# Kernel optimization log

Measured on AMD Instinct MI355X. Metric: run time of the kernel, lower is better.

## Reference

```python
import jax, jax.numpy as jnp
import numpy as np

N_NODES = 100000
N_EDGES = 1600000
N_GRAPHS = 256
IN_DIM, HID = 30, 40

def setup_inputs() -> dict:
    key = jax.random.key(0)
    ks = jax.random.split(key, 12)
    x = jax.random.normal(ks[0], (N_NODES, IN_DIM), dtype=jnp.float32)
    edge_index = jax.random.randint(ks[1], (2, N_EDGES), 0, N_NODES, dtype=jnp.int64)
    batch = jnp.sort(jax.random.randint(ks[2], (N_NODES,), 0, N_GRAPHS, dtype=jnp.int64))
    def glorot(k, shape):
        lim = float(np.sqrt(6.0 / (shape[0] + shape[1])))
        return jax.random.uniform(k, shape, dtype=jnp.float32, minval=-lim, maxval=lim)
    return {
        'x': x, 'edge_index': edge_index, 'batch': batch,
        'W1': glorot(ks[3], (IN_DIM, HID)), 'b1': jnp.zeros((HID,), jnp.float32),
        'W2': glorot(ks[4], (HID, HID)),    'b2': jnp.zeros((HID,), jnp.float32),
        'W3': glorot(ks[5], (HID, HID)),    'b3': jnp.zeros((HID,), jnp.float32),
        'lin_w': glorot(ks[6], (HID, 1)),   'lin_b': jnp.zeros((1,), jnp.float32),
    }

def _gcn_layer(x, src, dst, norm, W, b, n_nodes):
    # x: [N, Fin] -> [N, Fout]; fused gather-matmul-scatter form of GCNConv
    h = x @ W                                   # dense transform first (Fout small)
    msg = h[src] * norm[:, None]                # [E+N, Fout] gather + edge scale
    out = jax.ops.segment_sum(msg, dst, num_segments=n_nodes)
    return out + b

def reference(x, edge_index, batch, W1, b1, W2, b2, W3, b3, lin_w, lin_b):
    n = x.shape[0]
    loops = jnp.arange(n, dtype=edge_index.dtype)
    src = jnp.concatenate([edge_index[0], loops])  # add self loops (GCNConv default)
    dst = jnp.concatenate([edge_index[1], loops])
    deg = jax.ops.segment_sum(jnp.ones_like(dst, dtype=x.dtype), dst, num_segments=n)
    dinv = jax.lax.rsqrt(jnp.maximum(deg, 1.0))    # deg >= 1 thanks to self loops
    norm = dinv[src] * dinv[dst]

    h = jax.nn.relu(_gcn_layer(x, src, dst, norm, W1, b1, n))  # dropout inactive (eval)
    h = jax.nn.relu(_gcn_layer(h, src, dst, norm, W2, b2, n))
    h = jax.nn.relu(_gcn_layer(h, src, dst, norm, W3, b3, n))

    # global_mean_pool over graphs
    g_sum = jax.ops.segment_sum(h, batch, num_segments=N_GRAPHS)
    cnt = jax.ops.segment_sum(jnp.ones((n,), h.dtype), batch, num_segments=N_GRAPHS)
    g = g_sum / jnp.maximum(cnt, 1.0)[:, None]
    return g @ lin_w + lin_b                      # [N_GRAPHS, 1]
```

## Files before the change

### kernel.cpp

```cpp
#include <hip/hip_runtime.h>

#define HID 40
#define RBKT 196
#define BSH 9
#define CAP 12288
#define EPB 4096


__device__ inline unsigned pack2_bf16(float a, float b) {
    unsigned ua = __float_as_uint(a);
    unsigned ub = __float_as_uint(b);
    ua = (ua + 0x7fffu + ((ua >> 16) & 1u)) >> 16;
    ub = (ub + 0x7fffu + ((ub >> 16) & 1u)) & 0xffff0000u;
    return ua | ub;
}

__device__ inline void acc8_bf16(float* acc, uint4 v) {
    acc[0] += __uint_as_float(v.x << 16);
    acc[1] += __uint_as_float(v.x & 0xffff0000u);
    acc[2] += __uint_as_float(v.y << 16);
    acc[3] += __uint_as_float(v.y & 0xffff0000u);
    acc[4] += __uint_as_float(v.z << 16);
    acc[5] += __uint_as_float(v.z & 0xffff0000u);
    acc[6] += __uint_as_float(v.w << 16);
    acc[7] += __uint_as_float(v.w & 0xffff0000u);
}

__global__ void clear_kernel(int* __restrict__ bucket_cnt, float* __restrict__ g_sum, int G) {
    int t = blockIdx.x * blockDim.x + threadIdx.x;
    if (t < RBKT) bucket_cnt[t] = 0;
    if (t < G) g_sum[t] = 0.f;
}


__global__ __launch_bounds__(256) void binA_kernel(
        const int* __restrict__ esrc, const int* __restrict__ edst, int E,
        int* __restrict__ bucket_cnt, int* __restrict__ bucket_data) {
    __shared__ int cnt_l[RBKT];
    __shared__ int base_l[RBKT];
    int t = threadIdx.x;
    for (int b = t; b < RBKT; b += 256) cnt_l[b] = 0;
    __syncthreads();
    int e0 = blockIdx.x * EPB;
    int e1 = min(e0 + EPB, E);
    for (int e = e0 + t; e < e1; e += 256) {
        atomicAdd(&cnt_l[edst[e] >> BSH], 1);
    }
    __syncthreads();
    for (int b = t; b < RBKT; b += 256) {
        int c = cnt_l[b];
        base_l[b] = (c > 0) ? atomicAdd(&bucket_cnt[b], c) : 0;
        cnt_l[b] = 0;
    }
    __syncthreads();
    for (int e = e0 + t; e < e1; e += 256) {
        int d = edst[e];
        int s = esrc[e];
        int b = d >> BSH;
        int off = base_l[b] + atomicAdd(&cnt_l[b], 1);
        if (off < CAP) bucket_data[(size_t)b * CAP + off] = (s << BSH) | (d & 511);
    }
}

__global__ void scan_buckets_kernel(const int* __restrict__ cnt, int* __restrict__ base) {
    __shared__ int s[256];
    int t = threadIdx.x;
    int c = (t < RBKT) ? min(cnt[t], CAP) : 0;
    s[t] = c;
    __syncthreads();
    for (int off = 1; off < 256; off <<= 1) {
        int y = (t >= off) ? s[t - off] : 0;
        __syncthreads();
        s[t] += y;
        __syncthreads();
    }
    if (t < RBKT) base[t] = s[t] - c;
    if (t == RBKT - 1) base[RBKT] = s[t];
}

__global__ __launch_bounds__(256) void buildB_kernel(
        const int* __restrict__ bucket_cnt, const int* __restrict__ bucket_base,
        const int* __restrict__ bucket_data,
        int* __restrict__ rowptr, int* __restrict__ csr,
        float* __restrict__ dinv, int n) {
    __shared__ int deg_l[512];
    __shared__ int off_l[512];
    __shared__ int ps[256];
    int r = blockIdx.x;
    int t = threadIdx.x;
    int cnt = min(bucket_cnt[r], CAP);
    int base = bucket_base[r];
    int node0 = r << BSH;
    int nr = min(512, n - node0);
    for (int i = t; i < 512; i += 256) deg_l[i] = 0;
    __syncthreads();
    const int* data = bucket_data + (size_t)r * CAP;
    for (int e = t; e < cnt; e += 256) atomicAdd(&deg_l[data[e] & 511], 1);
    __syncthreads();
    int a0 = deg_l[2 * t], a1 = deg_l[2 * t + 1];
    ps[t] = a0 + a1;
    __syncthreads();
    for (int off = 1; off < 256; off <<= 1) {
        int y = (t >= off) ? ps[t - off] : 0;
        __syncthreads();
        ps[t] += y;
        __syncthreads();
    }
    int excl = ps[t] - (a0 + a1);
    off_l[2 * t] = excl;
    off_l[2 * t + 1] = excl + a0;
    __syncthreads();
    for (int i = t; i < nr; i += 256) {
        rowptr[node0 + i] = base + off_l[i];
        dinv[node0 + i] = rsqrtf((float)(deg_l[i] + 1));
    }
    if (r == RBKT - 1 && t == 0) rowptr[n] = base + cnt;
    __syncthreads();
    for (int e = t; e < cnt; e += 256) {
        int v = data[e];
        int p = atomicAdd(&off_l[v & 511], 1);
        csr[base + p] = v >> BSH;
    }
}


__global__ __launch_bounds__(256) void scale_bf16_kernel(
        const float* __restrict__ x, const float* __restrict__ dinv,
        unsigned* __restrict__ xs, int n) {
    int t = blockIdx.x * blockDim.x + threadIdx.x;
    int i = t >> 4, p = t & 15;
    if (i >= n) return;
    float a = 0.f, b = 0.f;
    if (p < 15) {
        float d = dinv[i];
        a = x[i * 30 + 2 * p] * d;
        b = x[i * 30 + 2 * p + 1] * d;
    }
    xs[(size_t)i * 16 + p] = pack2_bf16(a, b);
}

template <int INF, int TPN, int OUTF, bool POOL>
__global__ __launch_bounds__(64 * TPN) void fused_layer_kernel(
        const unsigned* __restrict__ xs, const int* __restrict__ rowptr,
        const int* __restrict__ csr, const float* __restrict__ dinv,
        const float* __restrict__ W, const float* __restrict__ bias,
        const float* __restrict__ lin_w, const int* __restrict__ batch,
        unsigned* __restrict__ gout, float* __restrict__ g_sum, int n) {
    constexpr int NT  = 64 * TPN;
    constexpr int STR = 8 * TPN + 1;
    constexpr int OPF = OUTF / TPN;
    __shared__ float Ws[INF * OUTF];
    __shared__ float aggs[64 * STR];
    __shared__ float lw[POOL ? OUTF : 1];
    __shared__ float sarr[POOL ? NT : 1];
    const int tid = threadIdx.x;
    for (int t = tid; t < INF * OUTF; t += NT) Ws[t] = W[t];
    if (POOL) {
        for (int t = tid; t < OUTF; t += NT) lw[t] = lin_w[t];
    }
    const int node_l = tid / TPN, q = tid - node_l * TPN;
    const int node = blockIdx.x * 64 + node_l;
    const bool valid = (node < n);
    if (valid) {
        const uint4* tab = reinterpret_cast<const uint4*>(xs);
        float acc[8];
        {
            uint4 v = tab[(size_t)node * TPN + q];
            acc[0] = __uint_as_float(v.x << 16);
            acc[1] = __uint_as_float(v.x & 0xffff0000u);
            acc[2] = __uint_as_float(v.y << 16);
            acc[3] = __uint_as_float(v.y & 0xffff0000u);
            acc[4] = __uint_as_float(v.z << 16);
            acc[5] = __uint_as_float(v.z & 0xffff0000u);
            acc[6] = __uint_as_float(v.w << 16);
            acc[7] = __uint_as_float(v.w & 0xffff0000u);
        }
        int e0 = rowptr[node], e1 = rowptr[node + 1];
        int e = e0;
        for (; e + 4 <= e1; e += 4) {
            int s0 = csr[e], s1 = csr[e + 1], s2 = csr[e + 2], s3 = csr[e + 3];
            uint4 v0 = tab[(size_t)s0 * TPN + q];
            uint4 v1 = tab[(size_t)s1 * TPN + q];
            uint4 v2 = tab[(size_t)s2 * TPN + q];
            uint4 v3 = tab[(size_t)s3 * TPN + q];
            acc8_bf16(acc, v0);
            acc8_bf16(acc, v1);
            acc8_bf16(acc, v2);
            acc8_bf16(acc, v3);
        }
        for (; e < e1; e++) {
            acc8_bf16(acc, tab[(size_t)csr[e] * TPN + q]);
        }
        float d = dinv[node];
        float* ar = &aggs[node_l * STR + q * 8];
        #pragma unroll
        for (int j = 0; j < 8; j++) ar[j] = acc[j] * d;
    }
    __syncthreads();
    if (POOL) sarr[tid] = 0.f;
    if (valid) {
        const float* arow = &aggs[node_l * STR];
        float acc2[OPF];
        #pragma unroll
        for (int j = 0; j < OPF; j++) acc2[j] = 0.f;
        for (int k = 0; k < INF; k++) {
            float xk = arow[k];
            #pragma unroll
            for (int j = 0; j < OPF; j++) acc2[j] += xk * Ws[k * OUTF + q * OPF + j];
        }
        if (!POOL) {
            float scale = dinv[node];
            unsigned* orow = gout + (size_t)node * (OUTF / 2) + q * (OPF / 2);
            #pragma unroll
            for (int j = 0; j < OPF / 2; j++) {
                int f = q * OPF + 2 * j;
                float v0 = fmaxf(acc2[2 * j] + bias[f], 0.f) * scale;
                float v1 = fmaxf(acc2[2 * j + 1] + bias[f + 1], 0.f) * scale;
                orow[j] = pack2_bf16(v0, v1);
            }
        } else {
            float s = 0.f;
            #pragma unroll
            for (int j = 0; j < OPF; j++) {
                int f = q * OPF + j;
                s += fmaxf(acc2[j] + bias[f], 0.f) * lw[f];
            }
            sarr[tid] = s;
        }
    }
    if (POOL) {
        __syncthreads();
        if (tid < 64) {
            float s = 0.f;
            #pragma unroll
            for (int q2 = 0; q2 < TPN; q2++) s += sarr[tid * TPN + q2];
            int node2 = blockIdx.x * 64 + tid;
            bool v2 = (node2 < n);
            int g = batch[v2 ? node2 : (n - 1)];
            if (!v2) s = 0.f;
            int g0 = __shfl(g, 0, 64);
            if (__all(g == g0)) {
                #pragma unroll
                for (int off = 32; off > 0; off >>= 1) s += __shfl_xor(s, off, 64);
                if (tid == 0) atomicAdd(&g_sum[g0], s);
            } else {
                if (v2) atomicAdd(&g_sum[g], s);
            }
        }
    }
}

__global__ void finalize_kernel(const float* __restrict__ g_sum,
                                const int* __restrict__ batch,
                                const float* __restrict__ lin_b,
                                float* __restrict__ out, int n, int G) {
    int b = blockIdx.x * blockDim.x + threadIdx.x;
    if (b >= G) return;
    int lo = 0, hi = n;
    while (lo < hi) { int m = (lo + hi) >> 1; if (batch[m] < b) lo = m + 1; else hi = m; }
    int lo2 = lo, hi2 = n;
    while (lo2 < hi2) { int m = (lo2 + hi2) >> 1; if (batch[m] < b + 1) lo2 = m + 1; else hi2 = m; }
    int cnt = lo2 - lo;
    out[b] = g_sum[b] / (float)(cnt > 0 ? cnt : 1) + lin_b[0];
}


static inline size_t align_up(size_t v, size_t a) { return (v + a - 1) / a * a; }

extern "C" void kernel_launch(void* const* d_in, const int* in_sizes, int n_in,
                              void* d_out, int out_size, void* d_ws, size_t ws_size,
                              hipStream_t stream) {
    const float* x      = (const float*)d_in[0];
    const int*   esrc   = (const int*)d_in[1];
    const int*   batch  = (const int*)d_in[2];
    const float* W1     = (const float*)d_in[3];
    const float* b1     = (const float*)d_in[4];
    const float* W2     = (const float*)d_in[5];
    const float* b2     = (const float*)d_in[6];
    const float* W3     = (const float*)d_in[7];
    const float* b3     = (const float*)d_in[8];
    const float* lin_w  = (const float*)d_in[9];
    const float* lin_b  = (const float*)d_in[10];
    float* out = (float*)d_out;

    const int n = in_sizes[0] / 30;
    const int E = in_sizes[1] / 2;
    const int G = out_size;
    const int* edst = esrc + E;

    char* w = (char*)d_ws;
    size_t off = 0;
    auto take = [&](size_t bytes) { size_t o = off; off = align_up(off + bytes, 256); return (void*)(w + o); };
    int*      bucket_cnt  = (int*)take((size_t)RBKT * 4);
    int*      bucket_base = (int*)take((size_t)(RBKT + 1) * 4);
    int*      rowptr      = (int*)take((size_t)(n + 1) * 4);
    float*    dinv        = (float*)take((size_t)n * 4);
    int*      csr         = (int*)take((size_t)E * 4);
    float*    g_sum       = (float*)take((size_t)G * 4);
    size_t bd = (size_t)RBKT * CAP * 4;
    size_t x1 = (size_t)n * 16 * 4;
    void* shared_region = take(bd > x1 ? bd : x1);
    int*      bucket_data = (int*)shared_region;
    unsigned* xs1         = (unsigned*)shared_region;
    unsigned* tbA         = (unsigned*)take((size_t)n * 20 * 4);
    unsigned* tbB         = (unsigned*)take((size_t)n * 20 * 4);
    (void)ws_size;

    clear_kernel<<<1, 256, 0, stream>>>(bucket_cnt, g_sum, G);

    binA_kernel<<<(E + EPB - 1) / EPB, 256, 0, stream>>>(esrc, edst, E, bucket_cnt, bucket_data);
    scan_buckets_kernel<<<1, 256, 0, stream>>>(bucket_cnt, bucket_base);
    buildB_kernel<<<RBKT, 256, 0, stream>>>(bucket_cnt, bucket_base, bucket_data,
                                            rowptr, csr, dinv, n);

    int nblk = (n + 63) / 64;

    scale_bf16_kernel<<<((size_t)n * 16 + 255) / 256, 256, 0, stream>>>(x, dinv, xs1, n);
    fused_layer_kernel<30, 4, HID, false><<<nblk, 256, 0, stream>>>(
        xs1, rowptr, csr, dinv, W1, b1, nullptr, nullptr, tbA, nullptr, n);
    fused_layer_kernel<HID, 5, HID, false><<<nblk, 320, 0, stream>>>(
        tbA, rowptr, csr, dinv, W2, b2, nullptr, nullptr, tbB, nullptr, n);
    fused_layer_kernel<HID, 5, HID, true><<<nblk, 320, 0, stream>>>(
        tbB, rowptr, csr, dinv, W3, b3, lin_w, batch, nullptr, g_sum, n);

    finalize_kernel<<<1, 256, 0, stream>>>(g_sum, batch, lin_b, out, n, G);
}
```

Before: 216.1 us.

## Split bf16 hidden table into 64B lo and 16B hi arrays with edge-split hi gather

The 40-feature bf16 node table (80 bytes per row) is split into a 32-feature array (64 B rows) and an 8-feature array (16 B rows). Layers 2 and 3 then gather the lo part with 4 threads per node and the hi part by splitting each node's edge list across the 4 threads, reducing partial sums in shared memory. The aim is aligned, cache-line-friendly gathers and 256-thread blocks instead of 320. csr/rowptr loads and output stores are made nontemporal. The cost is an extra shared-memory reduction and barrier, plus a second csr pass per node.

```diff
diff --git a/kernel.cpp b/kernel.cpp
--- a/kernel.cpp
+++ b/kernel.cpp
@@ -25,6 +25,9 @@
     acc[6] += __uint_as_float(v.w << 16);
     acc[7] += __uint_as_float(v.w & 0xffff0000u);
 }
+
+__device__ inline int ldnt(const int* p) { return __builtin_nontemporal_load(p); }
+__device__ inline void stnt(unsigned* p, unsigned v) { __builtin_nontemporal_store(v, p); }
 
 __global__ void clear_kernel(int* __restrict__ bucket_cnt, float* __restrict__ g_sum, int G) {
     int t = blockIdx.x * blockDim.x + threadIdx.x;
@@ -139,33 +142,41 @@
     xs[(size_t)i * 16 + p] = pack2_bf16(a, b);
 }
 
-template <int INF, int TPN, int OUTF, bool POOL>
-__global__ __launch_bounds__(64 * TPN) void fused_layer_kernel(
-        const unsigned* __restrict__ xs, const int* __restrict__ rowptr,
-        const int* __restrict__ csr, const float* __restrict__ dinv,
+template <int INF_LO, bool HAS_HI, bool POOL>
+__global__ __launch_bounds__(256) void fused_layer_kernel(
+        const unsigned* __restrict__ xs_lo, const unsigned* __restrict__ xs_hi,
+        const int* __restrict__ rowptr, const int* __restrict__ csr,
+        const float* __restrict__ dinv,
         const float* __restrict__ W, const float* __restrict__ bias,
         const float* __restrict__ lin_w, const int* __restrict__ batch,
-        unsigned* __restrict__ gout, float* __restrict__ g_sum, int n) {
-    constexpr int NT  = 64 * TPN;
-    constexpr int STR = 8 * TPN + 1;
-    constexpr int OPF = OUTF / TPN;
+        unsigned* __restrict__ go_lo, unsigned* __restrict__ go_hi,
+        float* __restrict__ g_sum, int n) {
+    constexpr int INF  = INF_LO + (HAS_HI ? 8 : 0);
+    constexpr int OUTF = 40;
+    constexpr int OPF  = 10;
     __shared__ float Ws[INF * OUTF];
-    __shared__ float aggs[64 * STR];
+    __shared__ float aggs[64 * 41];
+    __shared__ float part[HAS_HI ? 64 * 33 : 1];
     __shared__ float lw[POOL ? OUTF : 1];
-    __shared__ float sarr[POOL ? NT : 1];
+    __shared__ float sarr[POOL ? 256 : 1];
     const int tid = threadIdx.x;
-    for (int t = tid; t < INF * OUTF; t += NT) Ws[t] = W[t];
-    if (POOL) {
-        for (int t = tid; t < OUTF; t += NT) lw[t] = lin_w[t];
-    }
-    const int node_l = tid / TPN, q = tid - node_l * TPN;
-    const int node = blockIdx.x * 64 + node_l;
+    for (int t = tid; t < INF * OUTF; t += 256) Ws[t] = W[t];
+    if (POOL && tid < OUTF) lw[tid] = lin_w[tid];
+    const int nl = tid >> 2, q = tid & 3;
+    const int node = blockIdx.x * 64 + nl;
     const bool valid = (node < n);
+    int e0 = 0, e1 = 0;
+    float d = 0.f;
     if (valid) {
-        const uint4* tab = reinterpret_cast<const uint4*>(xs);
+        e0 = ldnt(&rowptr[node]);
+        e1 = ldnt(&rowptr[node + 1]);
+        d = dinv[node];
+    }
+    if (valid) {
+        const uint4* tab = reinterpret_cast<const uint4*>(xs_lo);
         float acc[8];
         {
-            uint4 v = tab[(size_t)node * TPN + q];
+            uint4 v = tab[(size_t)node * 4 + q];
             acc[0] = __uint_as_float(v.x << 16);
             acc[1] = __uint_as_float(v.x & 0xffff0000u);
             acc[2] = __uint_as_float(v.y << 16);
@@ -175,31 +186,79 @@
             acc[6] = __uint_as_float(v.w << 16);
             acc[7] = __uint_as_float(v.w & 0xffff0000u);
         }
-        int e0 = rowptr[node], e1 = rowptr[node + 1];
         int e = e0;
         for (; e + 4 <= e1; e += 4) {
-            int s0 = csr[e], s1 = csr[e + 1], s2 = csr[e + 2], s3 = csr[e + 3];
-            uint4 v0 = tab[(size_t)s0 * TPN + q];
-            uint4 v1 = tab[(size_t)s1 * TPN + q];
-            uint4 v2 = tab[(size_t)s2 * TPN + q];
-            uint4 v3 = tab[(size_t)s3 * TPN + q];
+            int s0 = ldnt(&csr[e]);
+            int s1 = ldnt(&csr[e + 1]);
+            int s2 = ldnt(&csr[e + 2]);
+            int s3 = ldnt(&csr[e + 3]);
+            uint4 v0 = tab[(size_t)s0 * 4 + q];
+            uint4 v1 = tab[(size_t)s1 * 4 + q];
+            uint4 v2 = tab[(size_t)s2 * 4 + q];
+            uint4 v3 = tab[(size_t)s3 * 4 + q];
             acc8_bf16(acc, v0);
             acc8_bf16(acc, v1);
             acc8_bf16(acc, v2);
             acc8_bf16(acc, v3);
         }
         for (; e < e1; e++) {
-            acc8_bf16(acc, tab[(size_t)csr[e] * TPN + q]);
-        }
-        float d = dinv[node];
-        float* ar = &aggs[node_l * STR + q * 8];
+            acc8_bf16(acc, tab[(size_t)ldnt(&csr[e]) * 4 + q]);
+        }
+        float* ar = &aggs[nl * 41 + q * 8];
         #pragma unroll
         for (int j = 0; j < 8; j++) ar[j] = acc[j] * d;
     }
-    __syncthreads();
+    if (HAS_HI && valid) {
+        const uint4* tabh = reinterpret_cast<const uint4*>(xs_hi);
+        float acc[8];
+        if (q == 0) {
+            uint4 v = tabh[node];
+            acc[0] = __uint_as_float(v.x << 16);
+            acc[1] = __uint_as_float(v.x & 0xffff0000u);
+            acc[2] = __uint_as_float(v.y << 16);
+            acc[3] = __uint_as_float(v.y & 0xffff0000u);
+            acc[4] = __uint_as_float(v.z << 16);
+            acc[5] = __uint_as_float(v.z & 0xffff0000u);
+            acc[6] = __uint_as_float(v.w << 16);
+            acc[7] = __uint_as_float(v.w & 0xffff0000u);
+        } else {
+            #pragma unroll
+            for (int j = 0; j < 8; j++) acc[j] = 0.f;
+        }
+        int len = e1 - e0;
+        int b0 = e0 + ((len * q) >> 2);
+        int b1 = e0 + ((len * (q + 1)) >> 2);
+        int e = b0;
+        for (; e + 2 <= b1; e += 2) {
+            int s0 = ldnt(&csr[e]);
+            int s1 = ldnt(&csr[e + 1]);
+            uint4 v0 = tabh[s0];
+            uint4 v1 = tabh[s1];
+            acc8_bf16(acc, v0);
+            acc8_bf16(acc, v1);
+        }
+        if (e < b1) acc8_bf16(acc, tabh[ldnt(&csr[e])]);
+        float* pr = &part[nl * 33 + q * 8];
+        #pragma unroll
+        for (int j = 0; j < 8; j++) pr[j] = acc[j];
+    }
+    __syncthreads();
+    if (HAS_HI) {
+        if (valid) {
+            float s0 = 0.f, s1 = 0.f;
+            #pragma unroll
+            for (int p = 0; p < 4; p++) {
+                s0 += part[nl * 33 + p * 8 + 2 * q];
+                s1 += part[nl * 33 + p * 8 + 2 * q + 1];
+            }
+            aggs[nl * 41 + 32 + 2 * q] = s0 * d;
+            aggs[nl * 41 + 32 + 2 * q + 1] = s1 * d;
+        }
+        __syncthreads();
+    }
     if (POOL) sarr[tid] = 0.f;
     if (valid) {
-        const float* arow = &aggs[node_l * STR];
+        const float* arow = &aggs[nl * 41];
         float acc2[OPF];
         #pragma unroll
         for (int j = 0; j < OPF; j++) acc2[j] = 0.f;
@@ -209,14 +268,17 @@
             for (int j = 0; j < OPF; j++) acc2[j] += xk * Ws[k * OUTF + q * OPF + j];
         }
         if (!POOL) {
-            float scale = dinv[node];
-            unsigned* orow = gout + (size_t)node * (OUTF / 2) + q * (OPF / 2);
+            unsigned* lo_row = go_lo + (size_t)node * 16;
+            unsigned* hi_row = go_hi + (size_t)node * 4;
             #pragma unroll
             for (int j = 0; j < OPF / 2; j++) {
                 int f = q * OPF + 2 * j;
-                float v0 = fmaxf(acc2[2 * j] + bias[f], 0.f) * scale;
-                float v1 = fmaxf(acc2[2 * j + 1] + bias[f + 1], 0.f) * scale;
-                orow[j] = pack2_bf16(v0, v1);
+                float v0 = fmaxf(acc2[2 * j] + bias[f], 0.f) * d;
+                float v1 = fmaxf(acc2[2 * j + 1] + bias[f + 1], 0.f) * d;
+                unsigned u = pack2_bf16(v0, v1);
+                int ui = q * 5 + j;
+                if (ui < 16) stnt(&lo_row[ui], u);
+                else         stnt(&hi_row[ui - 16], u);
             }
         } else {
             float s = 0.f;
@@ -231,9 +293,7 @@
     if (POOL) {
         __syncthreads();
         if (tid < 64) {
-            float s = 0.f;
-            #pragma unroll
-            for (int q2 = 0; q2 < TPN; q2++) s += sarr[tid * TPN + q2];
+            float s = sarr[tid * 4] + sarr[tid * 4 + 1] + sarr[tid * 4 + 2] + sarr[tid * 4 + 3];
             int node2 = blockIdx.x * 64 + tid;
             bool v2 = (node2 < n);
             int g = batch[v2 ? node2 : (n - 1)];
@@ -302,8 +362,10 @@
     void* shared_region = take(bd > x1 ? bd : x1);
     int*      bucket_data = (int*)shared_region;
     unsigned* xs1         = (unsigned*)shared_region;
-    unsigned* tbA         = (unsigned*)take((size_t)n * 20 * 4);
-    unsigned* tbB         = (unsigned*)take((size_t)n * 20 * 4);
+    unsigned* tbA_lo      = (unsigned*)take((size_t)n * 16 * 4);
+    unsigned* tbA_hi      = (unsigned*)take((size_t)n * 4 * 4);
+    unsigned* tbB_lo      = (unsigned*)take((size_t)n * 16 * 4);
+    unsigned* tbB_hi      = (unsigned*)take((size_t)n * 4 * 4);
     (void)ws_size;
 
     clear_kernel<<<1, 256, 0, stream>>>(bucket_cnt, g_sum, G);
@@ -316,12 +378,15 @@
     int nblk = (n + 63) / 64;
 
     scale_bf16_kernel<<<((size_t)n * 16 + 255) / 256, 256, 0, stream>>>(x, dinv, xs1, n);
-    fused_layer_kernel<30, 4, HID, false><<<nblk, 256, 0, stream>>>(
-        xs1, rowptr, csr, dinv, W1, b1, nullptr, nullptr, tbA, nullptr, n);
-    fused_layer_kernel<HID, 5, HID, false><<<nblk, 320, 0, stream>>>(
-        tbA, rowptr, csr, dinv, W2, b2, nullptr, nullptr, tbB, nullptr, n);
-    fused_layer_kernel<HID, 5, HID, true><<<nblk, 320, 0, stream>>>(
-        tbB, rowptr, csr, dinv, W3, b3, lin_w, batch, nullptr, g_sum, n);
+    fused_layer_kernel<30, false, false><<<nblk, 256, 0, stream>>>(
+        xs1, nullptr, rowptr, csr, dinv, W1, b1, nullptr, nullptr,
+        tbA_lo, tbA_hi, nullptr, n);
+    fused_layer_kernel<32, true, false><<<nblk, 256, 0, stream>>>(
+        tbA_lo, tbA_hi, rowptr, csr, dinv, W2, b2, nullptr, nullptr,
+        tbB_lo, tbB_hi, nullptr, n);
+    fused_layer_kernel<32, true, true><<<nblk, 256, 0, stream>>>(
+        tbB_lo, tbB_hi, rowptr, csr, dinv, W3, b3, lin_w, batch,
+        nullptr, nullptr, g_sum, n);
 
     finalize_kernel<<<1, 256, 0, stream>>>(g_sum, batch, lin_b, out, n, G);
 }
```

Result: slower. 335.2 us (+55.1%).

## Process nodes in degree-sorted order within each graph to balance wavefronts

Applied to the files above, without the earlier changes.

Adds a counting sort of nodes keyed by (graph id, clamped in-degree): a histogram, a single-block scan and an atomic scatter build a permutation. The three fused GCN layer kernels then walk nodes through this permutation, so the lanes of a wavefront get similar edge counts and graph-level pooling still sees mostly uniform graph ids per wavefront. The goal is less divergence and load imbalance in the gather loop. The cost is three extra small kernel launches, an extra indirection per node, and scattered per-node reads and writes of rowptr, dinv and the output rows.

```diff
diff --git a/kernel.cpp b/kernel.cpp
--- a/kernel.cpp
+++ b/kernel.cpp
@@ -5,6 +5,7 @@
 #define BSH 9
 #define CAP 12288
 #define EPB 4096
+#define NKEY 16384
 
 
 __device__ inline unsigned pack2_bf16(float a, float b) {
@@ -26,10 +27,12 @@
     acc[7] += __uint_as_float(v.w & 0xffff0000u);
 }
 
-__global__ void clear_kernel(int* __restrict__ bucket_cnt, float* __restrict__ g_sum, int G) {
+__global__ void clear_kernel(int* __restrict__ bucket_cnt, float* __restrict__ g_sum,
+                             int* __restrict__ ghist, int G) {
     int t = blockIdx.x * blockDim.x + threadIdx.x;
     if (t < RBKT) bucket_cnt[t] = 0;
     if (t < G) g_sum[t] = 0.f;
+    if (t < NKEY) ghist[t] = 0;
 }
 
 
@@ -124,6 +127,56 @@
 }
 
 
+__global__ void sort_hist_kernel(const int* __restrict__ rowptr, const int* __restrict__ batch,
+                                 int* __restrict__ ghist, int n) {
+    int i = blockIdx.x * blockDim.x + threadIdx.x;
+    if (i >= n) return;
+    int deg = min(rowptr[i + 1] - rowptr[i], 63);
+    atomicAdd(&ghist[batch[i] * 64 + deg], 1);
+}
+
+__global__ void scan_kernel(const int* __restrict__ cnt, int* __restrict__ base, int m) {
+    __shared__ int ws[16];
+    __shared__ int carry;
+    int tid = threadIdx.x;
+    int lane = tid & 63, wid = tid >> 6;
+    if (tid == 0) carry = 0;
+    __syncthreads();
+    for (int b0 = 0; b0 < m; b0 += 1024) {
+        int i = b0 + tid;
+        int v = (i < m) ? cnt[i] : 0;
+        int x = v;
+        #pragma unroll
+        for (int off = 1; off < 64; off <<= 1) {
+            int y = __shfl_up(x, off, 64);
+            if (lane >= off) x += y;
+        }
+        if (lane == 63) ws[wid] = x;
+        __syncthreads();
+        if (tid == 0) {
+            int acc = carry;
+            #pragma unroll
+            for (int w2 = 0; w2 < 16; w2++) { int tt = ws[w2]; ws[w2] = acc; acc += tt; }
+            carry = acc;
+        }
+        __syncthreads();
+        if (i < m) base[i] = ws[wid] + (x - v);
+        __syncthreads();
+    }
+    if (tid == 0) base[m] = carry;
+}
+
+__global__ void sort_scatter_kernel(const int* __restrict__ rowptr, const int* __restrict__ batch,
+                                    int* __restrict__ gbase, int* __restrict__ perm, int n) {
+    int i = blockIdx.x * blockDim.x + threadIdx.x;
+    if (i >= n) return;
+    int deg = min(rowptr[i + 1] - rowptr[i], 63);
+    int key = batch[i] * 64 + deg;
+    int pos = atomicAdd(&gbase[key], 1);
+    perm[pos] = i;
+}
+
+
 __global__ __launch_bounds__(256) void scale_bf16_kernel(
         const float* __restrict__ x, const float* __restrict__ dinv,
         unsigned* __restrict__ xs, int n) {
@@ -143,6 +196,7 @@
 __global__ __launch_bounds__(64 * TPN) void fused_layer_kernel(
         const unsigned* __restrict__ xs, const int* __restrict__ rowptr,
         const int* __restrict__ csr, const float* __restrict__ dinv,
+        const int* __restrict__ perm,
         const float* __restrict__ W, const float* __restrict__ bias,
         const float* __restrict__ lin_w, const int* __restrict__ batch,
         unsigned* __restrict__ gout, float* __restrict__ g_sum, int n) {
@@ -159,8 +213,9 @@
         for (int t = tid; t < OUTF; t += NT) lw[t] = lin_w[t];
     }
     const int node_l = tid / TPN, q = tid - node_l * TPN;
-    const int node = blockIdx.x * 64 + node_l;
-    const bool valid = (node < n);
+    const int j = blockIdx.x * 64 + node_l;
+    const bool valid = (j < n);
+    const int node = perm[valid ? j : 0];
     if (valid) {
         const uint4* tab = reinterpret_cast<const uint4*>(xs);
         float acc[8];
@@ -194,7 +249,7 @@
         float d = dinv[node];
         float* ar = &aggs[node_l * STR + q * 8];
         #pragma unroll
-        for (int j = 0; j < 8; j++) ar[j] = acc[j] * d;
+        for (int jj = 0; jj < 8; jj++) ar[jj] = acc[jj] * d;
     }
     __syncthreads();
     if (POOL) sarr[tid] = 0.f;
@@ -202,28 +257,28 @@
         const float* arow = &aggs[node_l * STR];
         float acc2[OPF];
         #pragma unroll
-        for (int j = 0; j < OPF; j++) acc2[j] = 0.f;
+        for (int jj = 0; jj < OPF; jj++) acc2[jj] = 0.f;
         for (int k = 0; k < INF; k++) {
             float xk = arow[k];
             #pragma unroll
-            for (int j = 0; j < OPF; j++) acc2[j] += xk * Ws[k * OUTF + q * OPF + j];
+            for (int jj = 0; jj < OPF; jj++) acc2[jj] += xk * Ws[k * OUTF + q * OPF + jj];
         }
         if (!POOL) {
             float scale = dinv[node];
             unsigned* orow = gout + (size_t)node * (OUTF / 2) + q * (OPF / 2);
             #pragma unroll
-            for (int j = 0; j < OPF / 2; j++) {
-                int f = q * OPF + 2 * j;
-                float v0 = fmaxf(acc2[2 * j] + bias[f], 0.f) * scale;
-                float v1 = fmaxf(acc2[2 * j + 1] + bias[f + 1], 0.f) * scale;
-                orow[j] = pack2_bf16(v0, v1);
+            for (int jj = 0; jj < OPF / 2; jj++) {
+                int f = q * OPF + 2 * jj;
+                float v0 = fmaxf(acc2[2 * jj] + bias[f], 0.f) * scale;
+                float v1 = fmaxf(acc2[2 * jj + 1] + bias[f + 1], 0.f) * scale;
+                orow[jj] = pack2_bf16(v0, v1);
             }
         } else {
             float s = 0.f;
             #pragma unroll
-            for (int j = 0; j < OPF; j++) {
-                int f = q * OPF + j;
-                s += fmaxf(acc2[j] + bias[f], 0.f) * lw[f];
+            for (int jj = 0; jj < OPF; jj++) {
+                int f = q * OPF + jj;
+                s += fmaxf(acc2[jj] + bias[f], 0.f) * lw[f];
             }
             sarr[tid] = s;
         }
@@ -234,10 +289,11 @@
             float s = 0.f;
             #pragma unroll
             for (int q2 = 0; q2 < TPN; q2++) s += sarr[tid * TPN + q2];
-            int node2 = blockIdx.x * 64 + tid;
-            bool v2 = (node2 < n);
-            int g = batch[v2 ? node2 : (n - 1)];
-            if (!v2) s = 0.f;
+            int j2 = blockIdx.x * 64 + tid;
+            bool v2 = (j2 < n);
+            int node2 = perm[v2 ? j2 : 0];
+            int g = batch[node2];
+            if (!v2) { s = 0.f; g = batch[perm[n - 1]]; }
             int g0 = __shfl(g, 0, 64);
             if (__all(g == g0)) {
                 #pragma unroll
@@ -297,6 +353,9 @@
     float*    dinv        = (float*)take((size_t)n * 4);
     int*      csr         = (int*)take((size_t)E * 4);
     float*    g_sum       = (float*)take((size_t)G * 4);
+    int*      ghist       = (int*)take((size_t)NKEY * 4);
+    int*      gbase       = (int*)take((size_t)(NKEY + 1) * 4);
+    int*      perm        = (int*)take((size_t)n * 4);
     size_t bd = (size_t)RBKT * CAP * 4;
     size_t x1 = (size_t)n * 16 * 4;
     void* shared_region = take(bd > x1 ? bd : x1);
@@ -306,22 +365,26 @@
     unsigned* tbB         = (unsigned*)take((size_t)n * 20 * 4);
     (void)ws_size;
 
-    clear_kernel<<<1, 256, 0, stream>>>(bucket_cnt, g_sum, G);
+    clear_kernel<<<(NKEY + 255) / 256, 256, 0, stream>>>(bucket_cnt, g_sum, ghist, G);
 
     binA_kernel<<<(E + EPB - 1) / EPB, 256, 0, stream>>>(esrc, edst, E, bucket_cnt, bucket_data);
     scan_buckets_kernel<<<1, 256, 0, stream>>>(bucket_cnt, bucket_base);
     buildB_kernel<<<RBKT, 256, 0, stream>>>(bucket_cnt, bucket_base, bucket_data,
                                             rowptr, csr, dinv, n);
 
+    sort_hist_kernel<<<(n + 255) / 256, 256, 0, stream>>>(rowptr, batch, ghist, n);
+    scan_kernel<<<1, 1024, 0, stream>>>(ghist, gbase, NKEY);
+    sort_scatter_kernel<<<(n + 255) / 256, 256, 0, stream>>>(rowptr, batch, gbase, perm, n);
+
     int nblk = (n + 63) / 64;
 
     scale_bf16_kernel<<<((size_t)n * 16 + 255) / 256, 256, 0, stream>>>(x, dinv, xs1, n);
     fused_layer_kernel<30, 4, HID, false><<<nblk, 256, 0, stream>>>(
-        xs1, rowptr, csr, dinv, W1, b1, nullptr, nullptr, tbA, nullptr, n);
+        xs1, rowptr, csr, dinv, perm, W1, b1, nullptr, nullptr, tbA, nullptr, n);
     fused_layer_kernel<HID, 5, HID, false><<<nblk, 320, 0, stream>>>(
-        tbA, rowptr, csr, dinv, W2, b2, nullptr, nullptr, tbB, nullptr, n);
+        tbA, rowptr, csr, dinv, perm, W2, b2, nullptr, nullptr, tbB, nullptr, n);
     fused_layer_kernel<HID, 5, HID, true><<<nblk, 320, 0, stream>>>(
-        tbB, rowptr, csr, dinv, W3, b3, lin_w, batch, nullptr, g_sum, n);
+        tbB, rowptr, csr, dinv, perm, W3, b3, lin_w, batch, nullptr, g_sum, n);
 
     finalize_kernel<<<1, 256, 0, stream>>>(g_sum, batch, lin_b, out, n, G);
 }
```

Result: slower. 256.2 us (+18.6%).

## Split CSR neighbor lists by source half to improve gather locality

Applied to the files above, without the earlier changes.

The CSR build now partitions each node's neighbors into sources from the lower half and the upper half of the node range, and records a mid pointer per node. The layer kernels gather the low-half neighbors first, then the high-half ones. The intent is that, across a wave, gathers at any moment touch a narrower region of the feature table, which should improve L2/MALL hit rates. The cost is extra shared-memory atomics in the build, one more per-node load, and two loop tails per node instead of one.

```diff
diff --git a/kernel.cpp b/kernel.cpp
--- a/kernel.cpp
+++ b/kernel.cpp
@@ -81,10 +81,12 @@
 __global__ __launch_bounds__(256) void buildB_kernel(
         const int* __restrict__ bucket_cnt, const int* __restrict__ bucket_base,
         const int* __restrict__ bucket_data,
-        int* __restrict__ rowptr, int* __restrict__ csr,
-        float* __restrict__ dinv, int n) {
+        int* __restrict__ rowptr, int* __restrict__ mid, int* __restrict__ csr,
+        float* __restrict__ dinv, int n, int half) {
     __shared__ int deg_l[512];
-    __shared__ int off_l[512];
+    __shared__ int deg_lo[512];
+    __shared__ int off_lo[512];
+    __shared__ int off_hi[512];
     __shared__ int ps[256];
     int r = blockIdx.x;
     int t = threadIdx.x;
@@ -92,10 +94,14 @@
     int base = bucket_base[r];
     int node0 = r << BSH;
     int nr = min(512, n - node0);
-    for (int i = t; i < 512; i += 256) deg_l[i] = 0;
+    for (int i = t; i < 512; i += 256) { deg_l[i] = 0; deg_lo[i] = 0; }
     __syncthreads();
     const int* data = bucket_data + (size_t)r * CAP;
-    for (int e = t; e < cnt; e += 256) atomicAdd(&deg_l[data[e] & 511], 1);
+    for (int e = t; e < cnt; e += 256) {
+        int v = data[e];
+        atomicAdd(&deg_l[v & 511], 1);
+        if ((v >> BSH) < half) atomicAdd(&deg_lo[v & 511], 1);
+    }
     __syncthreads();
     int a0 = deg_l[2 * t], a1 = deg_l[2 * t + 1];
     ps[t] = a0 + a1;
@@ -107,19 +113,25 @@
         __syncthreads();
     }
     int excl = ps[t] - (a0 + a1);
-    off_l[2 * t] = excl;
-    off_l[2 * t + 1] = excl + a0;
+    off_lo[2 * t] = excl;
+    off_lo[2 * t + 1] = excl + a0;
+    off_hi[2 * t] = excl + deg_lo[2 * t];
+    off_hi[2 * t + 1] = excl + a0 + deg_lo[2 * t + 1];
     __syncthreads();
     for (int i = t; i < nr; i += 256) {
-        rowptr[node0 + i] = base + off_l[i];
+        int rp = base + off_lo[i];
+        rowptr[node0 + i] = rp;
+        mid[node0 + i] = rp + deg_lo[i];
         dinv[node0 + i] = rsqrtf((float)(deg_l[i] + 1));
     }
     if (r == RBKT - 1 && t == 0) rowptr[n] = base + cnt;
     __syncthreads();
     for (int e = t; e < cnt; e += 256) {
         int v = data[e];
-        int p = atomicAdd(&off_l[v & 511], 1);
-        csr[base + p] = v >> BSH;
+        int s = v >> BSH;
+        int d = v & 511;
+        int p = (s < half) ? atomicAdd(&off_lo[d], 1) : atomicAdd(&off_hi[d], 1);
+        csr[base + p] = s;
     }
 }
 
@@ -142,7 +154,8 @@
 template <int INF, int TPN, int OUTF, bool POOL>
 __global__ __launch_bounds__(64 * TPN) void fused_layer_kernel(
         const unsigned* __restrict__ xs, const int* __restrict__ rowptr,
-        const int* __restrict__ csr, const float* __restrict__ dinv,
+        const int* __restrict__ mid, const int* __restrict__ csr,
+        const float* __restrict__ dinv,
         const float* __restrict__ W, const float* __restrict__ bias,
         const float* __restrict__ lin_w, const int* __restrict__ batch,
         unsigned* __restrict__ gout, float* __restrict__ g_sum, int n) {
@@ -175,8 +188,22 @@
             acc[6] = __uint_as_float(v.w << 16);
             acc[7] = __uint_as_float(v.w & 0xffff0000u);
         }
-        int e0 = rowptr[node], e1 = rowptr[node + 1];
+        int e0 = rowptr[node], m = mid[node], e1 = rowptr[node + 1];
         int e = e0;
+        for (; e + 4 <= m; e += 4) {
+            int s0 = csr[e], s1 = csr[e + 1], s2 = csr[e + 2], s3 = csr[e + 3];
+            uint4 v0 = tab[(size_t)s0 * TPN + q];
+            uint4 v1 = tab[(size_t)s1 * TPN + q];
+            uint4 v2 = tab[(size_t)s2 * TPN + q];
+            uint4 v3 = tab[(size_t)s3 * TPN + q];
+            acc8_bf16(acc, v0);
+            acc8_bf16(acc, v1);
+            acc8_bf16(acc, v2);
+            acc8_bf16(acc, v3);
+        }
+        for (; e < m; e++) {
+            acc8_bf16(acc, tab[(size_t)csr[e] * TPN + q]);
+        }
         for (; e + 4 <= e1; e += 4) {
             int s0 = csr[e], s1 = csr[e + 1], s2 = csr[e + 2], s3 = csr[e + 3];
             uint4 v0 = tab[(size_t)s0 * TPN + q];
@@ -294,6 +321,7 @@
     int*      bucket_cnt  = (int*)take((size_t)RBKT * 4);
     int*      bucket_base = (int*)take((size_t)(RBKT + 1) * 4);
     int*      rowptr      = (int*)take((size_t)(n + 1) * 4);
+    int*      mid         = (int*)take((size_t)n * 4);
     float*    dinv        = (float*)take((size_t)n * 4);
     int*      csr         = (int*)take((size_t)E * 4);
     float*    g_sum       = (float*)take((size_t)G * 4);
@@ -311,17 +339,17 @@
     binA_kernel<<<(E + EPB - 1) / EPB, 256, 0, stream>>>(esrc, edst, E, bucket_cnt, bucket_data);
     scan_buckets_kernel<<<1, 256, 0, stream>>>(bucket_cnt, bucket_base);
     buildB_kernel<<<RBKT, 256, 0, stream>>>(bucket_cnt, bucket_base, bucket_data,
-                                            rowptr, csr, dinv, n);
+                                            rowptr, mid, csr, dinv, n, n / 2);
 
     int nblk = (n + 63) / 64;
 
     scale_bf16_kernel<<<((size_t)n * 16 + 255) / 256, 256, 0, stream>>>(x, dinv, xs1, n);
     fused_layer_kernel<30, 4, HID, false><<<nblk, 256, 0, stream>>>(
-        xs1, rowptr, csr, dinv, W1, b1, nullptr, nullptr, tbA, nullptr, n);
+        xs1, rowptr, mid, csr, dinv, W1, b1, nullptr, nullptr, tbA, nullptr, n);
     fused_layer_kernel<HID, 5, HID, false><<<nblk, 320, 0, stream>>>(
-        tbA, rowptr, csr, dinv, W2, b2, nullptr, nullptr, tbB, nullptr, n);
+        tbA, rowptr, mid, csr, dinv, W2, b2, nullptr, nullptr, tbB, nullptr, n);
     fused_layer_kernel<HID, 5, HID, true><<<nblk, 320, 0, stream>>>(
-        tbB, rowptr, csr, dinv, W3, b3, lin_w, batch, nullptr, g_sum, n);
+        tbB, rowptr, mid, csr, dinv, W3, b3, lin_w, batch, nullptr, g_sum, n);
 
     finalize_kernel<<<1, 256, 0, stream>>>(g_sum, batch, lin_b, out, n, G);
 }
```

After: 209.6 us. 3.0% less time.
